# Performance work log

Measured on AMD Instinct MI355X. Metric: run time of the kernel, lower is better.

The kernel has to match this reference:

```python
import jax, jax.numpy as jnp
import numpy as np
import math

EPS = 1e-5

def _ln(x, g, b):
    m = jnp.mean(x, axis=-1, keepdims=True)
    v = jnp.var(x, axis=-1, keepdims=True)
    return (x - m) * jax.lax.rsqrt(v + EPS) * g + b

def _rn_layer(x, W, g, b, A, Bb, Rw):
    # x: (B,S,in) -> (B,S,out). W: (out,in), A: (out,basis), Bb: (basis,out)
    S = x.shape[1]
    basis_dim = Bb.shape[0]
    n = _ln(x @ W.T, g, b)                      # (B,S,out)
    j = jnp.arange(S) % basis_dim               # (S,)
    Bv = Bb[j]                                  # (S,out)
    scal = jnp.einsum('bsd,sd->bs', n, Bv)      # (B,S)
    Av = A[:, j].T                              # (S,out)
    nf = scal[..., None] * Av                   # (B,S,out)
    res = x if Rw is None else x @ Rw.T
    return nf + res

def _ts_layer(x, M, g, b, P, Rw):
    # x: (B,S,in) -> (B,S,out). M: (out,in), P: (out,out,G)
    S = x.shape[1]
    D, _, G = P.shape
    t = _ln(x @ M.T, g, b)                      # (B,S,out)
    k = jnp.arange(S, dtype=jnp.float32)
    periods = (jnp.arange(D, dtype=jnp.float32)[:, None, None] * (D * G)
               + jnp.arange(D, dtype=jnp.float32)[None, :, None] * G
               + jnp.arange(G, dtype=jnp.float32)[None, None, :] + 2.0)  # (D,D,G)
    phi = jnp.cos(2.0 * math.pi * k[:, None, None, None] / periods)       # (S,D,D,G)
    # Nk[b,s,i] = sum_{j,g} P[i,j,g] * t[b,s,j] * phi[s,i,j,g]
    Wp = jnp.einsum('ijg,sijg->sij', P, phi)    # (S,D,D)
    Nk = jnp.einsum('sij,bsj->bsi', Wp, t)      # (B,S,D)
    return Nk + x @ Rw.T

def setup_inputs() -> dict:
    key = jax.random.key(0)
    ks = jax.random.split(key, 16)
    B, S = 2, 2048
    d0, d1, d2 = 512, 64, 512        # input_dim, ts out, final out
    bas1, G, bas3 = 64, 8, 64
    u = lambda k, sh, a: jax.random.uniform(k, sh, jnp.float32, -a, a)
    inp = {
        'x':  jax.random.normal(ks[0], (B, S, d0), jnp.float32),
        # Layer 1: RN 512->512 (in==out -> no residual proj)
        'W1': u(ks[1], (d0, d0), 0.1),
        'g1': jnp.ones((d0,), jnp.float32),
        'b1': jnp.zeros((d0,), jnp.float32),
        'A1': u(ks[2], (d0, bas1), 0.1),
        'B1': u(ks[3], (bas1, d0), 0.1),
        # Layer 2: TS 512->64
        'M2': u(ks[4], (d1, d0), 0.5),
        'g2': jnp.ones((d1,), jnp.float32),
        'b2': jnp.zeros((d1,), jnp.float32),
        'P2': u(ks[5], (d1, d1, G), 0.1),
        'R2': u(ks[6], (d1, d0), 0.1),
        # Layer 3: RN 64->512
        'W3': u(ks[7], (d2, d1), 0.1),
        'g3': jnp.ones((d2,), jnp.float32),
        'b3': jnp.zeros((d2,), jnp.float32),
        'A3': u(ks[8], (d2, bas3), 0.1),
        'B3': u(ks[9], (bas3, d2), 0.1),
        'R3': u(ks[10], (d2, d1), 0.1),
    }
    return inp

def reference(x, W1, g1, b1, A1, B1, M2, g2, b2, P2, R2, W3, g3, b3, A3, B3, R3):
    h = _rn_layer(x, W1, g1, b1, A1, B1, None)   # (B,S,512), identity residual
    h = _ts_layer(h, M2, g2, b2, P2, R2)         # (B,S,64)
    h = _rn_layer(h, W3, g3, b3, A3, B3, R3)     # (B,S,512)
    return h
```

## Files before the change

kernel.cpp:

```cpp
#include <hip/hip_runtime.h>
#include <math.h>

#define SEQ  2048
#define ROWS 4096
#define D0   512
#define D1   64
#define C2S  524288

typedef short bf8 __attribute__((ext_vector_type(8)));
typedef float f4  __attribute__((ext_vector_type(4)));

__device__ __forceinline__ unsigned short f2bf(float f) {
    unsigned u = __float_as_uint(f);
    return (unsigned short)((u + 0x7fffu + ((u >> 16) & 1u)) >> 16);
}
__device__ __forceinline__ float bf2f(unsigned short u) {
    return __uint_as_float((unsigned)u << 16);
}
__device__ __forceinline__ void hilo(float f, unsigned short& h, unsigned short& l) {
    h = f2bf(f);
    float fh = bf2f(h);
    l = f2bf(f - fh);
}
__device__ __forceinline__ void cv4h(unsigned short* dh, int idx, float4 v) {
    ushort4 hv;
    hv.x = f2bf(v.x); hv.y = f2bf(v.y); hv.z = f2bf(v.z); hv.w = f2bf(v.w);
    *(ushort4*)(dh + idx) = hv;
}

__device__ __forceinline__ void async16(const void* g, void* l) {
    __builtin_amdgcn_global_load_lds(
        (const __attribute__((address_space(1))) unsigned int*)g,
        (__attribute__((address_space(3))) unsigned int*)l, 16, 0, 0);
}

__global__ __launch_bounds__(256) void convk(
        const float* __restrict__ x,  const float* __restrict__ W1,
        const float* __restrict__ M2, const float* __restrict__ R2,
        const float* __restrict__ W3, const float* __restrict__ R3,
        const float* __restrict__ A1, const float* __restrict__ A3,
        unsigned short* __restrict__ xh, unsigned short* __restrict__ xl,
        unsigned short* __restrict__ W1h,
        unsigned short* __restrict__ C2h,
        unsigned short* __restrict__ C3h,
        float* __restrict__ A3T,
        float* __restrict__ G2y, float* __restrict__ G2r) {
    __shared__ float sh[4][64];
    int c = blockIdx.x, tid = threadIdx.x;
    if (c < 1024) {
        int base = c * 2048 + tid * 4;
        float4 v0 = *(const float4*)(x + base);
        float4 v1 = *(const float4*)(x + base + 1024);
        ushort4 h, l;
        hilo(v0.x, h.x, l.x); hilo(v0.y, h.y, l.y);
        hilo(v0.z, h.z, l.z); hilo(v0.w, h.w, l.w);
        *(ushort4*)(xh + base) = h; *(ushort4*)(xl + base) = l;
        hilo(v1.x, h.x, l.x); hilo(v1.y, h.y, l.y);
        hilo(v1.z, h.z, l.z); hilo(v1.w, h.w, l.w);
        *(ushort4*)(xh + base + 1024) = h; *(ushort4*)(xl + base + 1024) = l;
    } else if (c < 1216) {
        const float* src; unsigned short* dh; int off;
        if      (c < 1152) { src = W1; dh = W1h;         off = c - 1024; }
        else if (c < 1168) { src = M2; dh = C2h;         off = c - 1152; }
        else if (c < 1184) { src = R2; dh = C2h + 32768; off = c - 1168; }
        else if (c < 1200) { src = W3; dh = C3h;         off = c - 1184; }
        else               { src = R3; dh = C3h + 32768; off = c - 1200; }
        int base = off * 2048 + tid * 4;
        cv4h(dh, base,        *(const float4*)(src + base));
        cv4h(dh, base + 1024, *(const float4*)(src + base + 1024));
    } else if (c < 1344) {
        int gid = (c - 1216) * 256 + tid;
        int i = gid >> 6, j = gid & 63;
        A3T[j * 512 + i] = A3[gid];
    } else {
        int jrow = (c - 1344) & 63;
        const float* wv = (c < 1408) ? (M2 + jrow * 512) : (R2 + jrow * 512);
        float* G = (c < 1408) ? G2y : G2r;
        int jm = tid & 63, q = tid >> 6;
        const float* ap = A1 + (q * 128) * 64 + jm;
        const float* wp = wv + q * 128;
        float acc = 0.f;
        for (int cc = 0; cc < 128; ++cc)
            acc = fmaf(ap[cc * 64], wp[cc], acc);
        sh[q][jm] = acc;
        __syncthreads();
        if (tid < 64)
            G[tid * 64 + jrow] = (sh[0][tid] + sh[1][tid]) + (sh[2][tid] + sh[3][tid]);
    }
}

__global__ __launch_bounds__(256, 3) void gemmw(
        const unsigned short* __restrict__ Ah, const unsigned short* __restrict__ Al,
        const unsigned short* __restrict__ Wh,
        float* __restrict__ Cf, unsigned short* __restrict__ Cb,
        int K, int Ks) {
    __shared__ __align__(16) unsigned short aH[4096];
    __shared__ __align__(16) unsigned short aL[4096];
    __shared__ __align__(16) unsigned short wHs[8192];
    const int tid = threadIdx.x;
    const int wv  = tid >> 6;
    const int ln  = tid & 63;
    const int lm  = ln & 15;
    const int lq  = ln >> 4;
    const int bm  = blockIdx.y * 64;
    const int bn  = blockIdx.x * 128;
    const int k0  = blockIdx.z * Ks;
    const bool alo = (bn >= 512);

    f4 acc[8] = {};

    for (int kt = 0; kt < Ks; kt += 64) {
        const int kg = k0 + kt;
        __syncthreads();
#pragma unroll
        for (int i = 0; i < 2; ++i) {
            int slot = i * 256 + wv * 64 + ln;
            int row  = slot >> 3;
            int ch   = (slot & 7) ^ (row & 7);
            size_t go = (size_t)(bm + row) * K + kg + ch * 8;
            async16(Ah + go, aH + slot * 8);
            if (alo) async16(Al + go, aL + slot * 8);
        }
#pragma unroll
        for (int i = 0; i < 4; ++i) {
            int slot = i * 256 + wv * 64 + ln;
            int row  = slot >> 3;
            int ch   = (slot & 7) ^ (row & 7);
            size_t go = (size_t)(bn + row) * K + kg + ch * 8;
            async16(Wh + go, wHs + slot * 8);
        }
        __syncthreads();

#pragma unroll
        for (int kk = 0; kk < 2; ++kk) {
            const int ck = kk * 4 + lq;
            bf8 a_h, a_l, b_h[8];
            {
                int r = wv * 16 + lm;
                a_h = *(const bf8*)(aH + r * 64 + ((ck ^ (r & 7)) * 8));
                if (alo)
                    a_l = *(const bf8*)(aL + r * 64 + ((ck ^ (r & 7)) * 8));
            }
#pragma unroll
            for (int u = 0; u < 8; ++u) {
                int rb = u * 16 + lm;
                b_h[u] = *(const bf8*)(wHs + rb * 64 + ((ck ^ (rb & 7)) * 8));
            }
#pragma unroll
            for (int u = 0; u < 8; ++u) {
                acc[u] = __builtin_amdgcn_mfma_f32_16x16x32_bf16(a_h, b_h[u], acc[u], 0, 0, 0);
                if (alo)
                    acc[u] = __builtin_amdgcn_mfma_f32_16x16x32_bf16(a_l, b_h[u], acc[u], 0, 0, 0);
            }
        }
    }

#pragma unroll
    for (int u = 0; u < 8; ++u) {
        int row = bm + wv * 16 + lq * 4;
        int col = bn + u * 16 + lm;
#pragma unroll
        for (int r = 0; r < 4; ++r) {
            float v = acc[u][r];
            if (col < 512)
                Cb[(size_t)blockIdx.z * ROWS * 512 + (size_t)(row + r) * 512 + col] = f2bf(v);
            else
                Cf[(size_t)blockIdx.z * ROWS * 128 + (size_t)(row + r) * 128 + (col - 512)] = v;
        }
    }
}

__global__ __launch_bounds__(256) void ptk(
        const unsigned short* __restrict__ C1b,
        const float* __restrict__ C2,
        const float* __restrict__ B1,
        const float* __restrict__ g1, const float* __restrict__ b1,
        const float* __restrict__ g2, const float* __restrict__ b2,
        const float* __restrict__ G2y, const float* __restrict__ G2r,
        float* __restrict__ t, float* __restrict__ rsum) {
    const int row = blockIdx.x * 4 + (threadIdx.x >> 6);
    const int l = threadIdx.x & 63;
    const int c = l * 8;
    const int jm = row & 63;
    const size_t rb0 = (size_t)row * 512 + c;
    ushort4 ua = *(const ushort4*)(C1b + rb0);
    ushort4 ub = *(const ushort4*)(C1b + rb0 + 4);
    ushort4 va = *(const ushort4*)(C1b + (size_t)ROWS * 512 + rb0);
    ushort4 vb = *(const ushort4*)(C1b + (size_t)ROWS * 512 + rb0 + 4);
    float y[8];
    y[0] = bf2f(ua.x) + bf2f(va.x); y[1] = bf2f(ua.y) + bf2f(va.y);
    y[2] = bf2f(ua.z) + bf2f(va.z); y[3] = bf2f(ua.w) + bf2f(va.w);
    y[4] = bf2f(ub.x) + bf2f(vb.x); y[5] = bf2f(ub.y) + bf2f(vb.y);
    y[6] = bf2f(ub.z) + bf2f(vb.z); y[7] = bf2f(ub.w) + bf2f(vb.w);
    float4 B0  = *(const float4*)(B1 + jm * 512 + c);
    float4 B1q = *(const float4*)(B1 + jm * 512 + c + 4);
    float4 gg0 = *(const float4*)(g1 + c), gg1 = *(const float4*)(g1 + c + 4);
    float4 bb0 = *(const float4*)(b1 + c), bb1 = *(const float4*)(b1 + c + 4);
    float Bv[8] = {B0.x, B0.y, B0.z, B0.w, B1q.x, B1q.y, B1q.z, B1q.w};
    float gv[8] = {gg0.x, gg0.y, gg0.z, gg0.w, gg1.x, gg1.y, gg1.z, gg1.w};
    float bv[8] = {bb0.x, bb0.y, bb0.z, bb0.w, bb1.x, bb1.y, bb1.z, bb1.w};
    float sum = 0.f, ssq = 0.f, S1 = 0.f, SU = 0.f, SBB = 0.f;
#pragma unroll
    for (int i = 0; i < 8; ++i) {
        float u = gv[i] * Bv[i];
        sum += y[i];
        ssq = fmaf(y[i], y[i], ssq);
        S1  = fmaf(y[i], u, S1);
        SU  += u;
        SBB = fmaf(bv[i], Bv[i], SBB);
    }
#pragma unroll
    for (int m = 1; m < 64; m <<= 1) {
        sum += __shfl_xor(sum, m, 64);
        ssq += __shfl_xor(ssq, m, 64);
        S1  += __shfl_xor(S1, m, 64);
        SU  += __shfl_xor(SU, m, 64);
        SBB += __shfl_xor(SBB, m, 64);
    }
    float mean = sum * (1.0f / 512.0f);
    float var  = ssq * (1.0f / 512.0f) - mean * mean;
    float rstd = rsqrtf(var + 1e-5f);
    float p = rstd * (S1 - mean * SU) + SBB;

    const size_t rb = (size_t)row * 128;
    float z  = C2[rb + l]      + C2[C2S + rb + l];
    float zr = C2[rb + 64 + l] + C2[C2S + rb + 64 + l];
    float v  = z  + p * G2y[jm * 64 + l];
    float rv = zr + p * G2r[jm * 64 + l];
    float s2 = v, q2 = v * v;
#pragma unroll
    for (int m = 1; m < 64; m <<= 1) {
        s2 += __shfl_xor(s2, m, 64);
        q2 += __shfl_xor(q2, m, 64);
    }
    float mean2 = s2 * (1.0f / 64.0f);
    float var2  = q2 * (1.0f / 64.0f) - mean2 * mean2;
    float rstd2 = rsqrtf(var2 + 1e-5f);
    t[row * 64 + l]    = (v - mean2) * rstd2 * g2[l] + b2[l];
    rsum[row * 64 + l] = rv;
}

__global__ __launch_bounds__(256) void tsk2(
        const float* __restrict__ t, const float* __restrict__ rsum,
        const float* __restrict__ P,
        unsigned short* __restrict__ Hh, unsigned short* __restrict__ Hl) {
    const int bid = blockIdx.x;
    const int i   = bid >> 3;
    const int sg  = bid & 7;
    const int w   = threadIdx.x >> 6;
    const int ln  = threadIdx.x & 63;
    const int s0  = sg * 256 + w * 64;
    const int idx = i * 64 + ln;
    const float* pp = P + idx * 8;
    const float sf0 = (float)s0;

    float k2c[8], ca[8], cb[8];
#pragma unroll
    for (int g = 0; g < 8; ++g) {
        float pf   = (float)(idx * 8 + g + 2);
        float invp = __builtin_amdgcn_rcpf(pf);
        k2c[g] = 2.0f * __builtin_amdgcn_cosf(invp);
        float q0 = floorf(sf0 * invp);
        float r0 = fmaf(-q0, pf, sf0);
        float f0 = r0 * invp; f0 -= floorf(f0);
        float c0 = __builtin_amdgcn_cosf(f0);
        float sf1 = sf0 + 1.0f;
        float q1 = floorf(sf1 * invp);
        float r1 = fmaf(-q1, pf, sf1);
        float f1 = r1 * invp; f1 -= floorf(f1);
        float c1 = __builtin_amdgcn_cosf(f1);
        float Pv = pp[g];
        ca[g] = Pv * c0;
        cb[g] = Pv * c1;
    }

    const int tb = s0 * 64 + ln;
    float t0c = t[tb], t1c = t[131072 + tb];
    float res0 = 0.f, res1 = 0.f;

    for (int st = 0; st < 64; st += 2) {
        float t0n  = t[tb + (st + 1) * 64];
        float t1n  = t[131072 + tb + (st + 1) * 64];
        float ws = ((ca[0] + ca[1]) + (ca[2] + ca[3]))
                 + ((ca[4] + ca[5]) + (ca[6] + ca[7]));
#pragma unroll
        for (int g = 0; g < 8; ++g) ca[g] = fmaf(k2c[g], cb[g], -ca[g]);
        float v0 = ws * t0c, v1 = ws * t1c;
#pragma unroll
        for (int m = 1; m < 64; m <<= 1) {
            v0 += __shfl_xor(v0, m, 64);
            v1 += __shfl_xor(v1, m, 64);
        }
        res0 = (ln == st) ? v0 : res0;
        res1 = (ln == st) ? v1 : res1;
        float t0n2 = t[tb + (st + 2) * 64];
        float t1n2 = t[131072 + tb + (st + 2) * 64];
        float ws2 = ((cb[0] + cb[1]) + (cb[2] + cb[3]))
                  + ((cb[4] + cb[5]) + (cb[6] + cb[7]));
#pragma unroll
        for (int g = 0; g < 8; ++g) cb[g] = fmaf(k2c[g], ca[g], -cb[g]);
        float v0b = ws2 * t0n, v1b = ws2 * t1n;
#pragma unroll
        for (int m = 1; m < 64; m <<= 1) {
            v0b += __shfl_xor(v0b, m, 64);
            v1b += __shfl_xor(v1b, m, 64);
        }
        res0 = (ln == st + 1) ? v0b : res0;
        res1 = (ln == st + 1) ? v1b : res1;
        t0c = t0n2; t1c = t1n2;
    }

    const int s = s0 + ln;
    {
        float v = res0 + rsum[(size_t)s * 64 + i];
        unsigned short h, l; hilo(v, h, l);
        Hh[(size_t)s * 64 + i] = h; Hl[(size_t)s * 64 + i] = l;
        float v1e = res1 + rsum[(size_t)(SEQ + s) * 64 + i];
        hilo(v1e, h, l);
        Hh[(size_t)(SEQ + s) * 64 + i] = h; Hl[(size_t)(SEQ + s) * 64 + i] = l;
    }
}

__global__ __launch_bounds__(256) void g3ln(
        const unsigned short* __restrict__ Hh, const unsigned short* __restrict__ Hl,
        const unsigned short* __restrict__ Wc3h,
        const float* __restrict__ g3, const float* __restrict__ b3,
        const float* __restrict__ B3, const float* __restrict__ A3T,
        float* __restrict__ outf) {
    __shared__ __align__(16) unsigned short aH[1024];
    __shared__ __align__(16) unsigned short aL[1024];
    __shared__ __align__(16) unsigned short wS[16384];
    __shared__ float cS[16 * 1024];
    const int tid = threadIdx.x;
    const int wv  = tid >> 6;
    const int ln  = tid & 63;
    const int lm  = ln & 15;
    const int lq  = ln >> 4;
    const int r0  = blockIdx.x * 16;

    {
        int slot = (wv & 1) * 64 + ln;
        int row  = slot >> 3;
        int ch   = (slot & 7) ^ (row & 7);
        size_t go = (size_t)(r0 + row) * 64 + ch * 8;
        if (wv < 2) async16(Hh + go, aH + slot * 8);
        else        async16(Hl + go, aL + slot * 8);
    }

    bf8 ah[2], al[2];
    for (int q = 0; q < 4; ++q) {
#pragma unroll
        for (int i = 0; i < 8; ++i) {
            int slot = i * 256 + tid;
            int lr   = slot >> 3;
            int ch   = (slot & 7) ^ (lr & 7);
            int grow = (lr >> 6) * 256 + q * 64 + (lr & 63);
            size_t go = (size_t)grow * 64 + ch * 8;
            async16(Wc3h + go, wS + slot * 8);
        }
        __syncthreads();
        if (q == 0) {
#pragma unroll
            for (int kk = 0; kk < 2; ++kk) {
                int ck = kk * 4 + lq;
                ah[kk] = *(const bf8*)(aH + lm * 64 + ((ck ^ (lm & 7)) * 8));
                al[kk] = *(const bf8*)(aL + lm * 64 + ((ck ^ (lm & 7)) * 8));
            }
        }
        f4 acc[4] = {};
#pragma unroll
        for (int kk = 0; kk < 2; ++kk) {
            int ck = kk * 4 + lq;
            bf8 bh[4];
#pragma unroll
            for (int u = 0; u < 4; ++u) {
                int lr = wv * 64 + u * 16 + lm;
                bh[u] = *(const bf8*)(wS + lr * 64 + ((ck ^ (lr & 7)) * 8));
            }
#pragma unroll
            for (int u = 0; u < 4; ++u) {
                acc[u] = __builtin_amdgcn_mfma_f32_16x16x32_bf16(ah[kk], bh[u], acc[u], 0, 0, 0);
                acc[u] = __builtin_amdgcn_mfma_f32_16x16x32_bf16(al[kk], bh[u], acc[u], 0, 0, 0);
            }
        }
#pragma unroll
        for (int u = 0; u < 4; ++u) {
            int col = wv * 256 + q * 64 + u * 16 + lm;
#pragma unroll
            for (int r = 0; r < 4; ++r)
                cS[(lq * 4 + r) * 1024 + col] = acc[u][r];
        }
        __syncthreads();
    }

    for (int rr = 0; rr < 4; ++rr) {
        int row  = wv * 4 + rr;
        int grow = r0 + row;
        int jm   = grow & 63;
        const float* Bp = B3  + jm * 512;
        const float* Ap = A3T + jm * 512;
        float sum = 0.f, ssq = 0.f, S1 = 0.f, SU = 0.f, SBB = 0.f;
#pragma unroll
        for (int k = 0; k < 8; ++k) {
            int col = ln + k * 64;
            float y  = cS[row * 1024 + col];
            float Bv = Bp[col];
            float gv = g3[col];
            float bv = b3[col];
            float u = gv * Bv;
            sum += y;
            ssq = fmaf(y, y, ssq);
            S1  = fmaf(y, u, S1);
            SU  += u;
            SBB = fmaf(bv, Bv, SBB);
        }
#pragma unroll
        for (int m = 1; m < 64; m <<= 1) {
            sum += __shfl_xor(sum, m, 64);
            ssq += __shfl_xor(ssq, m, 64);
            S1  += __shfl_xor(S1, m, 64);
            SU  += __shfl_xor(SU, m, 64);
            SBB += __shfl_xor(SBB, m, 64);
        }
        float mean = sum * (1.0f / 512.0f);
        float var  = ssq * (1.0f / 512.0f) - mean * mean;
        float rstd = rsqrtf(var + 1e-5f);
        float p = rstd * (S1 - mean * SU) + SBB;
#pragma unroll
        for (int k = 0; k < 8; ++k) {
            int col = ln + k * 64;
            float res = cS[row * 1024 + 512 + col];
            outf[(size_t)grow * 512 + col] = fmaf(p, Ap[col], res);
        }
    }
}

extern "C" void kernel_launch(void* const* d_in, const int* in_sizes, int n_in,
                              void* d_out, int out_size, void* d_ws, size_t ws_size,
                              hipStream_t stream) {
    (void)in_sizes; (void)n_in; (void)out_size; (void)ws_size;
    const float* x  = (const float*)d_in[0];
    const float* W1 = (const float*)d_in[1];
    const float* g1 = (const float*)d_in[2];
    const float* b1 = (const float*)d_in[3];
    const float* A1 = (const float*)d_in[4];
    const float* B1 = (const float*)d_in[5];
    const float* M2 = (const float*)d_in[6];
    const float* g2 = (const float*)d_in[7];
    const float* b2 = (const float*)d_in[8];
    const float* P2 = (const float*)d_in[9];
    const float* R2 = (const float*)d_in[10];
    const float* W3 = (const float*)d_in[11];
    const float* g3 = (const float*)d_in[12];
    const float* b3 = (const float*)d_in[13];
    const float* A3 = (const float*)d_in[14];
    const float* B3 = (const float*)d_in[15];
    const float* R3 = (const float*)d_in[16];

    float* ws = (float*)d_ws;
    float* C2   = ws;
    float* t    = ws + 4194304;
    float* rsum = ws + 4456448;
    float* G2y  = ws + 4718592;
    float* G2r  = ws + 4722688;
    float* A3T  = ws + 4751360;
    unsigned short* us = (unsigned short*)(ws + 4784128);
    unsigned short* xh   = us;
    unsigned short* xl   = us + 2097152;
    unsigned short* W1h  = us + 6291456;
    unsigned short* Wc2h = us + 6553600;
    unsigned short* Wc3h = us + 6619136;
    unsigned short* h2h  = us + 6684672;
    unsigned short* h2l  = us + 6946816;
    unsigned short* C1b  = us + 7208960;

    dim3 blk(256);

    convk<<<1472, blk, 0, stream>>>(x, W1, M2, R2, W3, R3, A1, A3,
                                    xh, xl, W1h, Wc2h, Wc3h, A3T, G2y, G2r);

    gemmw<<<dim3(5, 64, 2), blk, 0, stream>>>(xh, xl, W1h, C2, C1b, 512, 256);

    ptk<<<1024, blk, 0, stream>>>(C1b, C2, B1, g1, b1, g2, b2, G2y, G2r, t, rsum);

    tsk2<<<512, blk, 0, stream>>>(t, rsum, P2, h2h, h2l);

    g3ln<<<256, blk, 0, stream>>>(h2h, h2l, Wc3h, g3, b3, B3, A3T, (float*)d_out);
}
```

Baseline: 143.4 us.

## Fuse layer-1 LayerNorm statistics into GEMM epilogue and drop split-K

The first GEMM drops its split-K over two slices and uses 64-column tiles on a 10x64 grid. Its epilogue computes per-row partial sums, sums of squares and the B1-weighted projection instead of writing the full bf16 C1 matrix. The row-invariant SU and SBB dot products move into the conversion prologue kernel, so ptk only combines 8 partials per row. This removes the large C1 write and reread and the split-K reduction, in exchange for more blocks each doing a full K loop and a heavier epilogue with B1 gathers.

```diff
diff --git a/kernel.cpp b/kernel.cpp
--- a/kernel.cpp
+++ b/kernel.cpp
@@ -5,7 +5,6 @@
 #define ROWS 4096
 #define D0   512
 #define D1   64
-#define C2S  524288
 
 typedef short bf8 __attribute__((ext_vector_type(8)));
 typedef float f4  __attribute__((ext_vector_type(4)));
@@ -39,12 +38,15 @@
         const float* __restrict__ M2, const float* __restrict__ R2,
         const float* __restrict__ W3, const float* __restrict__ R3,
         const float* __restrict__ A1, const float* __restrict__ A3,
+        const float* __restrict__ g1, const float* __restrict__ b1,
+        const float* __restrict__ B1,
         unsigned short* __restrict__ xh, unsigned short* __restrict__ xl,
         unsigned short* __restrict__ W1h,
         unsigned short* __restrict__ C2h,
         unsigned short* __restrict__ C3h,
         float* __restrict__ A3T,
-        float* __restrict__ G2y, float* __restrict__ G2r) {
+        float* __restrict__ G2y, float* __restrict__ G2r,
+        float* __restrict__ SU1, float* __restrict__ SBB1) {
     __shared__ float sh[4][64];
     int c = blockIdx.x, tid = threadIdx.x;
     if (c < 1024) {
@@ -72,7 +74,7 @@
         int gid = (c - 1216) * 256 + tid;
         int i = gid >> 6, j = gid & 63;
         A3T[j * 512 + i] = A3[gid];
-    } else {
+    } else if (c < 1472) {
         int jrow = (c - 1344) & 63;
         const float* wv = (c < 1408) ? (M2 + jrow * 512) : (R2 + jrow * 512);
         float* G = (c < 1408) ? G2y : G2r;
@@ -86,31 +88,43 @@
         __syncthreads();
         if (tid < 64)
             G[tid * 64 + jrow] = (sh[0][tid] + sh[1][tid]) + (sh[2][tid] + sh[3][tid]);
-    }
-}
-
-__global__ __launch_bounds__(256, 3) void gemmw(
+    } else {
+        const float* vec = (c == 1472) ? g1 : b1;
+        float* dst = (c == 1472) ? SU1 : SBB1;
+        int jm = tid >> 2, q = tid & 3;
+        const float* bp = B1 + jm * 512 + q * 128;
+        const float* vp = vec + q * 128;
+        float acc = 0.f;
+        for (int cc = 0; cc < 128; ++cc)
+            acc = fmaf(bp[cc], vp[cc], acc);
+        sh[q][jm] = acc;
+        __syncthreads();
+        if (tid < 64)
+            dst[tid] = (sh[0][tid] + sh[1][tid]) + (sh[2][tid] + sh[3][tid]);
+    }
+}
+
+__global__ __launch_bounds__(256, 4) void gemmk(
         const unsigned short* __restrict__ Ah, const unsigned short* __restrict__ Al,
         const unsigned short* __restrict__ Wh,
-        float* __restrict__ Cf, unsigned short* __restrict__ Cb,
-        int K, int Ks) {
+        const float* __restrict__ g1, const float* __restrict__ B1,
+        float* __restrict__ C2, float* __restrict__ Ps) {
     __shared__ __align__(16) unsigned short aH[4096];
     __shared__ __align__(16) unsigned short aL[4096];
-    __shared__ __align__(16) unsigned short wHs[8192];
+    __shared__ __align__(16) unsigned short wHs[4096];
     const int tid = threadIdx.x;
     const int wv  = tid >> 6;
     const int ln  = tid & 63;
     const int lm  = ln & 15;
     const int lq  = ln >> 4;
     const int bm  = blockIdx.y * 64;
-    const int bn  = blockIdx.x * 128;
-    const int k0  = blockIdx.z * Ks;
+    const int bn  = blockIdx.x * 64;
     const bool alo = (bn >= 512);
-
-    f4 acc[8] = {};
-
-    for (int kt = 0; kt < Ks; kt += 64) {
-        const int kg = k0 + kt;
+    const int K = 512;
+
+    f4 acc[4] = {};
+
+    for (int kg = 0; kg < K; kg += 64) {
         __syncthreads();
 #pragma unroll
         for (int i = 0; i < 2; ++i) {
@@ -122,7 +136,7 @@
             if (alo) async16(Al + go, aL + slot * 8);
         }
 #pragma unroll
-        for (int i = 0; i < 4; ++i) {
+        for (int i = 0; i < 2; ++i) {
             int slot = i * 256 + wv * 64 + ln;
             int row  = slot >> 3;
             int ch   = (slot & 7) ^ (row & 7);
@@ -134,7 +148,7 @@
 #pragma unroll
         for (int kk = 0; kk < 2; ++kk) {
             const int ck = kk * 4 + lq;
-            bf8 a_h, a_l, b_h[8];
+            bf8 a_h, a_l, b_h[4];
             {
                 int r = wv * 16 + lm;
                 a_h = *(const bf8*)(aH + r * 64 + ((ck ^ (r & 7)) * 8));
@@ -142,12 +156,12 @@
                     a_l = *(const bf8*)(aL + r * 64 + ((ck ^ (r & 7)) * 8));
             }
 #pragma unroll
-            for (int u = 0; u < 8; ++u) {
+            for (int u = 0; u < 4; ++u) {
                 int rb = u * 16 + lm;
                 b_h[u] = *(const bf8*)(wHs + rb * 64 + ((ck ^ (rb & 7)) * 8));
             }
 #pragma unroll
-            for (int u = 0; u < 8; ++u) {
+            for (int u = 0; u < 4; ++u) {
                 acc[u] = __builtin_amdgcn_mfma_f32_16x16x32_bf16(a_h, b_h[u], acc[u], 0, 0, 0);
                 if (alo)
                     acc[u] = __builtin_amdgcn_mfma_f32_16x16x32_bf16(a_l, b_h[u], acc[u], 0, 0, 0);
@@ -155,78 +169,76 @@
         }
     }
 
-#pragma unroll
-    for (int u = 0; u < 8; ++u) {
-        int row = bm + wv * 16 + lq * 4;
-        int col = bn + u * 16 + lm;
-#pragma unroll
-        for (int r = 0; r < 4; ++r) {
-            float v = acc[u][r];
-            if (col < 512)
-                Cb[(size_t)blockIdx.z * ROWS * 512 + (size_t)(row + r) * 512 + col] = f2bf(v);
-            else
-                Cf[(size_t)blockIdx.z * ROWS * 128 + (size_t)(row + r) * 128 + (col - 512)] = v;
+    if (bn < 512) {
+        float s0a[4] = {0.f, 0.f, 0.f, 0.f};
+        float q0a[4] = {0.f, 0.f, 0.f, 0.f};
+        float s1a[4] = {0.f, 0.f, 0.f, 0.f};
+#pragma unroll
+        for (int u = 0; u < 4; ++u) {
+            int col = bn + u * 16 + lm;
+            float gv = g1[col];
+#pragma unroll
+            for (int r = 0; r < 4; ++r) {
+                float y = acc[u][r];
+                int jm = (bm + wv * 16 + lq * 4 + r) & 63;
+                s0a[r] += y;
+                q0a[r] = fmaf(y, y, q0a[r]);
+                s1a[r] = fmaf(y, gv * B1[jm * 512 + col], s1a[r]);
+            }
+        }
+#pragma unroll
+        for (int m = 1; m < 16; m <<= 1) {
+#pragma unroll
+            for (int r = 0; r < 4; ++r) {
+                s0a[r] += __shfl_xor(s0a[r], m, 64);
+                q0a[r] += __shfl_xor(q0a[r], m, 64);
+                s1a[r] += __shfl_xor(s1a[r], m, 64);
+            }
+        }
+        if (lm == 0) {
+#pragma unroll
+            for (int r = 0; r < 4; ++r) {
+                int row = bm + wv * 16 + lq * 4 + r;
+                size_t pb = ((size_t)blockIdx.x * ROWS + row) * 3;
+                Ps[pb]     = s0a[r];
+                Ps[pb + 1] = q0a[r];
+                Ps[pb + 2] = s1a[r];
+            }
+        }
+    } else {
+#pragma unroll
+        for (int u = 0; u < 4; ++u) {
+            int row = bm + wv * 16 + lq * 4;
+            int col = bn + u * 16 + lm;
+#pragma unroll
+            for (int r = 0; r < 4; ++r)
+                C2[(size_t)(row + r) * 128 + (col - 512)] = acc[u][r];
         }
     }
 }
 
 __global__ __launch_bounds__(256) void ptk(
-        const unsigned short* __restrict__ C1b,
-        const float* __restrict__ C2,
-        const float* __restrict__ B1,
-        const float* __restrict__ g1, const float* __restrict__ b1,
+        const float* __restrict__ Ps, const float* __restrict__ C2,
         const float* __restrict__ g2, const float* __restrict__ b2,
         const float* __restrict__ G2y, const float* __restrict__ G2r,
+        const float* __restrict__ SU1, const float* __restrict__ SBB1,
         float* __restrict__ t, float* __restrict__ rsum) {
     const int row = blockIdx.x * 4 + (threadIdx.x >> 6);
     const int l = threadIdx.x & 63;
-    const int c = l * 8;
     const int jm = row & 63;
-    const size_t rb0 = (size_t)row * 512 + c;
-    ushort4 ua = *(const ushort4*)(C1b + rb0);
-    ushort4 ub = *(const ushort4*)(C1b + rb0 + 4);
-    ushort4 va = *(const ushort4*)(C1b + (size_t)ROWS * 512 + rb0);
-    ushort4 vb = *(const ushort4*)(C1b + (size_t)ROWS * 512 + rb0 + 4);
-    float y[8];
-    y[0] = bf2f(ua.x) + bf2f(va.x); y[1] = bf2f(ua.y) + bf2f(va.y);
-    y[2] = bf2f(ua.z) + bf2f(va.z); y[3] = bf2f(ua.w) + bf2f(va.w);
-    y[4] = bf2f(ub.x) + bf2f(vb.x); y[5] = bf2f(ub.y) + bf2f(vb.y);
-    y[6] = bf2f(ub.z) + bf2f(vb.z); y[7] = bf2f(ub.w) + bf2f(vb.w);
-    float4 B0  = *(const float4*)(B1 + jm * 512 + c);
-    float4 B1q = *(const float4*)(B1 + jm * 512 + c + 4);
-    float4 gg0 = *(const float4*)(g1 + c), gg1 = *(const float4*)(g1 + c + 4);
-    float4 bb0 = *(const float4*)(b1 + c), bb1 = *(const float4*)(b1 + c + 4);
-    float Bv[8] = {B0.x, B0.y, B0.z, B0.w, B1q.x, B1q.y, B1q.z, B1q.w};
-    float gv[8] = {gg0.x, gg0.y, gg0.z, gg0.w, gg1.x, gg1.y, gg1.z, gg1.w};
-    float bv[8] = {bb0.x, bb0.y, bb0.z, bb0.w, bb1.x, bb1.y, bb1.z, bb1.w};
-    float sum = 0.f, ssq = 0.f, S1 = 0.f, SU = 0.f, SBB = 0.f;
-#pragma unroll
-    for (int i = 0; i < 8; ++i) {
-        float u = gv[i] * Bv[i];
-        sum += y[i];
-        ssq = fmaf(y[i], y[i], ssq);
-        S1  = fmaf(y[i], u, S1);
-        SU  += u;
-        SBB = fmaf(bv[i], Bv[i], SBB);
-    }
-#pragma unroll
-    for (int m = 1; m < 64; m <<= 1) {
-        sum += __shfl_xor(sum, m, 64);
-        ssq += __shfl_xor(ssq, m, 64);
-        S1  += __shfl_xor(S1, m, 64);
-        SU  += __shfl_xor(SU, m, 64);
-        SBB += __shfl_xor(SBB, m, 64);
+    float sum = 0.f, ssq = 0.f, S1 = 0.f;
+#pragma unroll
+    for (int bn = 0; bn < 8; ++bn) {
+        const float* pp = Ps + ((size_t)bn * ROWS + row) * 3;
+        sum += pp[0]; ssq += pp[1]; S1 += pp[2];
     }
     float mean = sum * (1.0f / 512.0f);
     float var  = ssq * (1.0f / 512.0f) - mean * mean;
     float rstd = rsqrtf(var + 1e-5f);
-    float p = rstd * (S1 - mean * SU) + SBB;
-
-    const size_t rb = (size_t)row * 128;
-    float z  = C2[rb + l]      + C2[C2S + rb + l];
-    float zr = C2[rb + 64 + l] + C2[C2S + rb + 64 + l];
-    float v  = z  + p * G2y[jm * 64 + l];
-    float rv = zr + p * G2r[jm * 64 + l];
+    float p = rstd * (S1 - mean * SU1[jm]) + SBB1[jm];
+
+    float v  = C2[(size_t)row * 128 + l]      + p * G2y[jm * 64 + l];
+    float rv = C2[(size_t)row * 128 + 64 + l] + p * G2r[jm * 64 + l];
     float s2 = v, q2 = v * v;
 #pragma unroll
     for (int m = 1; m < 64; m <<= 1) {
@@ -459,10 +471,13 @@
 
     float* ws = (float*)d_ws;
     float* C2   = ws;
+    float* Ps   = ws + 524288;
     float* t    = ws + 4194304;
     float* rsum = ws + 4456448;
     float* G2y  = ws + 4718592;
     float* G2r  = ws + 4722688;
+    float* SU1  = ws + 4726784;
+    float* SBB1 = ws + 4726912;
     float* A3T  = ws + 4751360;
     unsigned short* us = (unsigned short*)(ws + 4784128);
     unsigned short* xh   = us;
@@ -472,16 +487,16 @@
     unsigned short* Wc3h = us + 6619136;
     unsigned short* h2h  = us + 6684672;
     unsigned short* h2l  = us + 6946816;
-    unsigned short* C1b  = us + 7208960;
 
     dim3 blk(256);
 
-    convk<<<1472, blk, 0, stream>>>(x, W1, M2, R2, W3, R3, A1, A3,
-                                    xh, xl, W1h, Wc2h, Wc3h, A3T, G2y, G2r);
-
-    gemmw<<<dim3(5, 64, 2), blk, 0, stream>>>(xh, xl, W1h, C2, C1b, 512, 256);
-
-    ptk<<<1024, blk, 0, stream>>>(C1b, C2, B1, g1, b1, g2, b2, G2y, G2r, t, rsum);
+    convk<<<1474, blk, 0, stream>>>(x, W1, M2, R2, W3, R3, A1, A3, g1, b1, B1,
+                                    xh, xl, W1h, Wc2h, Wc3h, A3T,
+                                    G2y, G2r, SU1, SBB1);
+
+    gemmk<<<dim3(10, 64, 1), blk, 0, stream>>>(xh, xl, W1h, g1, B1, C2, Ps);
+
+    ptk<<<1024, blk, 0, stream>>>(Ps, C2, g2, b2, G2y, G2r, SU1, SBB1, t, rsum);
 
     tsk2<<<512, blk, 0, stream>>>(t, rsum, P2, h2h, h2l);
 
```

After: 147.5 us. 1.03x slower.
